# Performance work log

Measured on AMD Instinct MI355X. Metric: run time of the kernel, lower is better.

Reference implementation:

```python
import jax, jax.numpy as jnp
import numpy as np

B, N, T_IN, F_IN = 16, 30000, 6, 1
E = 120000          # edges per etype
N_ETYPES = 2        # etypes per graph (hg and tg each)
KT, LK = 3, 3
C1, C2 = 8, 11      # block channel sizes
HID = 128


def _conv2d(x, w, b):
    # x: [B,Cin,T,N], w: [Cout,Cin,kt,1] -> valid conv
    y = jax.lax.conv_general_dilated(x, w, window_strides=(1, 1), padding='VALID',
                                     dimension_numbers=('NCHW', 'OIHW', 'NCHW'))
    return y + b[None, :, None, None]


def _glu_tconv(x, w, b, c_out, x_align):
    # TemporalConvLayer with act='GLU'
    xc = _conv2d(x, w, b)
    return (xc[:, :c_out] + x_align) * jax.nn.sigmoid(xc[:, c_out:])


def _hetcheb(X, edges, W, bias):
    # Heterogeneous ChebConv (sum over edge types), lambda_max=2 => L_hat = -D^-1/2 A D^-1/2
    # X: [S,N,Cin], edges: [n_et,2,E] int32, W: [n_et,Lk,Cin,Cout], bias: [n_et,Cout]
    S, n, cin = X.shape
    Lk = W.shape[1]
    Xn = jnp.transpose(X, (1, 0, 2))  # [N,S,Cin]
    out = jnp.zeros((n, S, W.shape[-1]), X.dtype)
    for e in range(edges.shape[0]):
        src, dst = edges[e, 0], edges[e, 1]
        ones = jnp.ones(src.shape, X.dtype)
        deg_in = jnp.clip(jax.ops.segment_sum(ones, dst, num_segments=n), 1.0)
        deg_out = jnp.clip(jax.ops.segment_sum(ones, src, num_segments=n), 1.0)
        norm = jax.lax.rsqrt(deg_out)[src] * jax.lax.rsqrt(deg_in)[dst]  # [E]
        def prop(Tm):  # L_hat @ T = -(Ahat @ T); vectorized over all B*T slices at once
            Tf = Tm.reshape(n, S * cin)
            return -jax.ops.segment_sum(norm[:, None] * Tf[src], dst, num_segments=n).reshape(n, S, cin)
        Tkm2 = Xn
        Tkm1 = prop(Xn)
        z = jnp.einsum('nsc,cd->nsd', Tkm2, W[e, 0]) + jnp.einsum('nsc,cd->nsd', Tkm1, W[e, 1])
        for k in range(2, Lk):
            Tk = 2.0 * prop(Tkm1) - Tkm2
            z = z + jnp.einsum('nsc,cd->nsd', Tk, W[e, k])
            Tkm2, Tkm1 = Tkm1, Tk
        out = out + z + bias[e][None, None, :]
    return jnp.transpose(out, (1, 0, 2))  # [S,N,Cout]


def _block(x, hg_edges, tg_edges, align_fn, tw, tb, hW, hb, tW, tb2, c_out):
    # HetETAConvBlock (dropout = identity in eval)
    x_align = align_fn(x)[:, :, KT - 1:, :]
    x_t1 = _glu_tconv(x, tw, tb, c_out, x_align)          # [B,c_out,T',N]
    b_, c_, t_, n_ = x_t1.shape
    X = jnp.transpose(x_t1, (0, 2, 3, 1)).reshape(b_ * t_, n_, c_)  # batched slices
    xs = _hetcheb(X, hg_edges, hW, hb).reshape(b_, t_, n_, -1).transpose(0, 3, 1, 2)
    xt = _hetcheb(X, tg_edges, tW, tb2).reshape(b_, t_, n_, -1).transpose(0, 3, 1, 2)
    return jnp.concatenate([xs, xt], axis=1)              # [B,2*c_out,T',N]


def setup_inputs() -> dict:
    key = jax.random.key(0)
    ks = jax.random.split(key, 20)
    s = 0.1
    inp = {
        'x': jax.random.normal(ks[0], (B, N, T_IN, F_IN), jnp.float32),
        'hg_edges': jax.random.randint(ks[1], (N_ETYPES, 2, E), 0, N, jnp.int32),
        'tg_edges': jax.random.randint(ks[2], (N_ETYPES, 2, E), 0, N, jnp.int32),
        # block1: tconv GLU 1 -> 8 (out 2*8 channels)
        'tconv1_w': jax.random.normal(ks[3], (2 * C1, F_IN, KT, 1), jnp.float32) * s,
        'tconv1_b': jnp.zeros((2 * C1,), jnp.float32),
        'h1_W': jax.random.normal(ks[4], (N_ETYPES, LK, C1, C1), jnp.float32) * s,
        'h1_b': jnp.zeros((N_ETYPES, C1), jnp.float32),
        't1_W': jax.random.normal(ks[5], (N_ETYPES, LK, C1, C1), jnp.float32) * s,
        't1_b': jnp.zeros((N_ETYPES, C1), jnp.float32),
        # block2: align 16 -> 11 (conv1x1), tconv GLU 16 -> 11
        'align2_w': jax.random.normal(ks[6], (C2, 2 * C1, 1, 1), jnp.float32) * s,
        'align2_b': jnp.zeros((C2,), jnp.float32),
        'tconv2_w': jax.random.normal(ks[7], (2 * C2, 2 * C1, KT, 1), jnp.float32) * s,
        'tconv2_b': jnp.zeros((2 * C2,), jnp.float32),
        'h2_W': jax.random.normal(ks[8], (N_ETYPES, LK, C2, C2), jnp.float32) * s,
        'h2_b': jnp.zeros((N_ETYPES, C2), jnp.float32),
        't2_W': jax.random.normal(ks[9], (N_ETYPES, LK, C2, C2), jnp.float32) * s,
        't2_b': jnp.zeros((N_ETYPES, C2), jnp.float32),
        # output linear: 11*2*(6-2*(3-1)) = 44 -> HID
        'out_w': jax.random.normal(ks[10], (2 * C2 * (T_IN - 2 * (KT - 1)), HID), jnp.float32) * s,
        'out_b': jnp.zeros((HID,), jnp.float32),
    }
    return inp


def reference(x, hg_edges, tg_edges, tconv1_w, tconv1_b, h1_W, h1_b, t1_W, t1_b,
              align2_w, align2_b, tconv2_w, tconv2_b, h2_W, h2_b, t2_W, t2_b,
              out_w, out_b):
    x = jnp.transpose(x, (0, 3, 2, 1))  # [B,1,T,N]
    # block1: Align pads channels 1 -> 8
    align1 = lambda v: jnp.pad(v, ((0, 0), (0, C1 - F_IN), (0, 0), (0, 0)))
    x1 = _block(x, hg_edges, tg_edges, align1, tconv1_w, tconv1_b, h1_W, h1_b, t1_W, t1_b, C1)
    # block2: Align is 1x1 conv 16 -> 11
    align2 = lambda v: _conv2d(v, align2_w, align2_b)
    x2 = _block(x1, hg_edges, tg_edges, align2, tconv2_w, tconv2_b, h2_W, h2_b, t2_W, t2_b, C2)
    b_, c_, t_, n_ = x2.shape
    z = jnp.transpose(x2, (0, 3, 1, 2)).reshape(b_, n_, c_ * t_)  # [B,N,44]
    return z @ out_w + out_b  # [B,N,HID]
```

## Files before the change

kernel.cpp:

```cpp
#include <hip/hip_runtime.h>
#include <hip/hip_fp16.h>
#include <math.h>

#define EDGES 120000
#define NN    30000
#define NCH   118
#define T1SLOT 15360000

__device__ __forceinline__ float sigmoidf_(float x) { return 1.f / (1.f + __expf(-x)); }

union F4H8 { float4 v; __half h[8]; };
union F2H4 { float2 v; __half h[4]; };

__device__ __forceinline__ void unpack8(float4 v, float* f) {
  F4H8 u; u.v = v;
#pragma unroll
  for (int i = 0; i < 8; ++i) f[i] = __half2float(u.h[i]);
}
__device__ __forceinline__ float4 pack8(const float* f) {
  F4H8 u;
#pragma unroll
  for (int i = 0; i < 8; ++i) u.h[i] = __float2half(f[i]);
  return u.v;
}
__device__ __forceinline__ void unpack4(float2 v, float* f) {
  F2H4 u; u.v = v;
#pragma unroll
  for (int i = 0; i < 4; ++i) f[i] = __half2float(u.h[i]);
}
__device__ __forceinline__ float2 pack4(const float* f) {
  F2H4 u;
#pragma unroll
  for (int i = 0; i < 4; ++i) u.h[i] = __float2half(f[i]);
  return u.v;
}

#define CSR_STRIDE 270016
#define CSR_RP(base, l)   ((base) + (size_t)(l) * CSR_STRIDE)
#define CSR_PK(base, l)   ((const int2*)((base) + (size_t)(l) * CSR_STRIDE + 30016))
#define CSR_PKW(base, l)  ((int2*)((base) + (size_t)(l) * CSR_STRIDE + 30016))

__global__ void count_all_kernel(const int* __restrict__ hg, const int* __restrict__ tg,
                                 int* __restrict__ degO, int* __restrict__ degI) {
  int tid = blockIdx.x * blockDim.x + threadIdx.x;
  if (tid >= 4 * EDGES) return;
  int l = tid / EDGES, j = tid - l * EDGES;
  const int* G = (l < 2) ? hg : tg;
  const int* src = G + (size_t)(l & 1) * 2 * EDGES;
  const int* dst = src + EDGES;
  atomicAdd(&degO[l * NN + src[j]], 1);
  atomicAdd(&degI[l * NN + dst[j]], 1);
}

__global__ __launch_bounds__(256) void scan1_kernel(const int* __restrict__ degI,
                                                    int* __restrict__ csrBase,
                                                    int* __restrict__ partials) {
  int l = blockIdx.x / NCH, ch = blockIdx.x - l * NCH;
  int tid = threadIdx.x;
  int i = ch * 256 + tid;
  __shared__ int buf[256];
  int v = (i < NN) ? degI[l * NN + i] : 0;
  buf[tid] = v;
  __syncthreads();
  for (int off = 1; off < 256; off <<= 1) {
    int t = (tid >= off) ? buf[tid - off] : 0;
    __syncthreads();
    buf[tid] += t;
    __syncthreads();
  }
  int* rp = CSR_RP(csrBase, l);
  if (i < NN) rp[i + 1] = buf[tid];
  if (tid == 255) partials[l * NCH + ch] = buf[255];
}

__global__ __launch_bounds__(128) void scan2_kernel(int* __restrict__ partials) {
  __shared__ int buf[128];
  int tid = threadIdx.x;
  for (int l = 0; l < 4; ++l) {
    int v = (tid < NCH) ? partials[l * NCH + tid] : 0;
    buf[tid] = v;
    __syncthreads();
    for (int off = 1; off < 128; off <<= 1) {
      int t = (tid >= off) ? buf[tid - off] : 0;
      __syncthreads();
      buf[tid] += t;
      __syncthreads();
    }
    if (tid < NCH) partials[l * NCH + tid] = buf[tid] - v;
    __syncthreads();
  }
}

__global__ __launch_bounds__(256) void fixup_kernel(int* __restrict__ csrBase,
                                                    int* __restrict__ cursor,
                                                    const int* __restrict__ partials) {
  int l = blockIdx.x / NCH, ch = blockIdx.x - l * NCH;
  int i = ch * 256 + threadIdx.x;
  int* rp = CSR_RP(csrBase, l);
  int off = partials[l * NCH + ch];
  if (i < NN) {
    int val = rp[i + 1] + off;
    rp[i + 1] = val;
    if (i + 1 < NN) cursor[l * NN + i + 1] = val;
  }
  if (i == 0) { rp[0] = 0; cursor[l * NN] = 0; }
}

__global__ void fill_all_kernel(const int* __restrict__ hg, const int* __restrict__ tg,
                                const int* __restrict__ degO, const int* __restrict__ degI,
                                int* __restrict__ cursor, int* __restrict__ csrBase) {
  int tid = blockIdx.x * blockDim.x + threadIdx.x;
  if (tid >= 4 * EDGES) return;
  int l = tid / EDGES, j = tid - l * EDGES;
  const int* G = (l < 2) ? hg : tg;
  const int* src = G + (size_t)(l & 1) * 2 * EDGES;
  const int* dst = src + EDGES;
  int s = src[j], d = dst[j];
  int doo = degO[l * NN + s]; if (doo < 1) doo = 1;
  int dii = degI[l * NN + d]; if (dii < 1) dii = 1;
  float nm = rsqrtf((float)doo) * rsqrtf((float)dii);
  int p = atomicAdd(&cursor[l * NN + d], 1);
  CSR_PKW(csrBase, l)[p] = make_int2(s, __float_as_int(nm));
}

__global__ void glu1_kernel(const float* __restrict__ x, const float* __restrict__ w,
                            const float* __restrict__ b, __half* __restrict__ X1h) {
  int idx = blockIdx.x * blockDim.x + threadIdx.x;
  if (idx >= NN * 64) return;
  int n = idx >> 6, s = idx & 63;
  int bb = s >> 2, t = s & 3;
  const float* xb = x + ((long)bb * NN + n) * 6;
  float x0 = xb[t], x1 = xb[t + 1], x2 = xb[t + 2];
  float o[8];
#pragma unroll
  for (int c = 0; c < 8; ++c) {
    float p = w[c * 3 + 0] * x0 + w[c * 3 + 1] * x1 + w[c * 3 + 2] * x2 + b[c];
    float q = w[(c + 8) * 3 + 0] * x0 + w[(c + 8) * 3 + 1] * x1 + w[(c + 8) * 3 + 2] * x2 + b[c + 8];
    float al = (c == 0) ? x2 : 0.f;
    o[c] = (p + al) * sigmoidf_(q);
  }
  reinterpret_cast<float4*>(X1h)[idx] = pack8(o);
}

__global__ __launch_bounds__(256) void pull1_kernel(const int* __restrict__ csrBase,
                                                    const __half* __restrict__ Xh,
                                                    __half* __restrict__ T1hAll) {
  int gtid = blockIdx.x * 256 + threadIdx.x;
  int l = gtid / (NN * 64);
  int t = gtid - l * (NN * 64);
  int n = t >> 6, j = t & 63;
  const int* rp = CSR_RP(csrBase, l);
  const int2* pk = CSR_PK(csrBase, l);
  const float4* in4 = reinterpret_cast<const float4*>(Xh);
  float acc[8];
#pragma unroll
  for (int i = 0; i < 8; ++i) acc[i] = 0.f;
  int e = rp[n], end = rp[n + 1];
  for (; e + 4 <= end; e += 4) {
    int2 p0 = pk[e], p1 = pk[e + 1], p2 = pk[e + 2], p3 = pk[e + 3];
    float4 v0 = in4[(long)p0.x * 64 + j];
    float4 v1 = in4[(long)p1.x * 64 + j];
    float4 v2 = in4[(long)p2.x * 64 + j];
    float4 v3 = in4[(long)p3.x * 64 + j];
    float f[8];
    float n0 = __int_as_float(p0.y), n1 = __int_as_float(p1.y);
    float n2 = __int_as_float(p2.y), n3 = __int_as_float(p3.y);
    unpack8(v0, f);
#pragma unroll
    for (int i = 0; i < 8; ++i) acc[i] -= n0 * f[i];
    unpack8(v1, f);
#pragma unroll
    for (int i = 0; i < 8; ++i) acc[i] -= n1 * f[i];
    unpack8(v2, f);
#pragma unroll
    for (int i = 0; i < 8; ++i) acc[i] -= n2 * f[i];
    unpack8(v3, f);
#pragma unroll
    for (int i = 0; i < 8; ++i) acc[i] -= n3 * f[i];
  }
  for (; e < end; ++e) {
    int2 p = pk[e];
    float4 v = in4[(long)p.x * 64 + j];
    float nm = __int_as_float(p.y);
    float f[8];
    unpack8(v, f);
#pragma unroll
    for (int i = 0; i < 8; ++i) acc[i] -= nm * f[i];
  }
  reinterpret_cast<float4*>(T1hAll)[(size_t)l * (T1SLOT / 8) + t] = pack8(acc);
}

__global__ __launch_bounds__(256) void cheb1_kernel(const int* __restrict__ csrBase,
    const __half* __restrict__ Xh, const __half* __restrict__ T1hAll,
    const float* __restrict__ Whg, const float* __restrict__ bhg,
    const float* __restrict__ Wtg, const float* __restrict__ btg,
    __half* __restrict__ Pbase) {
  constexpr int C = 8, CC = 64;
  __shared__ float wx[CC], w1[CC], w2[CC], bs[C];
  int gtid = blockIdx.x * 256 + threadIdx.x;
  int l = gtid / (NN * 64);
  int tid = gtid - l * (NN * 64);
  int g = l >> 1, et = l & 1;
  const float* W = (g ? Wtg : Whg) + et * 3 * CC;
  const float* bias = (g ? btg : bhg) + et * C;
  for (int i = threadIdx.x; i < CC; i += 256) {
    float w0v = W[i], w1v = W[CC + i], w2v = W[2 * CC + i];
    wx[i] = w0v - w2v; w1[i] = w1v; w2[i] = -2.f * w2v;
  }
  if (threadIdx.x < C) bs[threadIdx.x] = bias[threadIdx.x];
  __syncthreads();
  int n = tid >> 6, s = tid & 63;
  const int* rp = CSR_RP(csrBase, l);
  const int2* pk = CSR_PK(csrBase, l);
  const float4* T4 = reinterpret_cast<const float4*>(T1hAll + (size_t)l * T1SLOT);
  float acc[C];
#pragma unroll
  for (int c = 0; c < C; ++c) acc[c] = 0.f;
  int e = rp[n], end = rp[n + 1];
  for (; e + 4 <= end; e += 4) {
    int2 p0 = pk[e], p1 = pk[e + 1], p2 = pk[e + 2], p3 = pk[e + 3];
    float4 v0 = T4[(long)p0.x * 64 + s];
    float4 v1 = T4[(long)p1.x * 64 + s];
    float4 v2 = T4[(long)p2.x * 64 + s];
    float4 v3 = T4[(long)p3.x * 64 + s];
    float n0 = __int_as_float(p0.y), n1 = __int_as_float(p1.y);
    float n2 = __int_as_float(p2.y), n3 = __int_as_float(p3.y);
    float f[8];
    unpack8(v0, f);
#pragma unroll
    for (int c = 0; c < C; ++c) acc[c] += n0 * f[c];
    unpack8(v1, f);
#pragma unroll
    for (int c = 0; c < C; ++c) acc[c] += n1 * f[c];
    unpack8(v2, f);
#pragma unroll
    for (int c = 0; c < C; ++c) acc[c] += n2 * f[c];
    unpack8(v3, f);
#pragma unroll
    for (int c = 0; c < C; ++c) acc[c] += n3 * f[c];
  }
  for (; e < end; ++e) {
    int2 p = pk[e];
    float4 v = T4[(long)p.x * 64 + s];
    float nm = __int_as_float(p.y);
    float f[8];
    unpack8(v, f);
#pragma unroll
    for (int c = 0; c < C; ++c) acc[c] += nm * f[c];
  }
  float xv[C], tv[C];
  unpack8(reinterpret_cast<const float4*>(Xh)[tid], xv);
  unpack8(T4[tid], tv);
  float z[C];
#pragma unroll
  for (int d = 0; d < C; ++d) z[d] = bs[d];
#pragma unroll
  for (int c = 0; c < C; ++c) {
    float xc = xv[c], tc = tv[c], ac = acc[c];
#pragma unroll
    for (int d = 0; d < C; ++d)
      z[d] += xc * wx[c * C + d] + tc * w1[c * C + d] + ac * w2[c * C + d];
  }
  reinterpret_cast<float4*>(Pbase)[(size_t)l * (T1SLOT / 8) + tid] = pack8(z);
}

__global__ __launch_bounds__(256) void glu2_kernel(const __half* __restrict__ P,
                                                   const float* __restrict__ w2, const float* __restrict__ b2,
                                                   const float* __restrict__ aw, const float* __restrict__ ab,
                                                   __half* __restrict__ X2nh) {
  __shared__ float w2s[22 * 16 * 3], b2s[22], aws[11 * 16], abs_[11];
  for (int i = threadIdx.x; i < 22 * 16 * 3; i += 256) w2s[i] = w2[i];
  if (threadIdx.x < 22) b2s[threadIdx.x] = b2[threadIdx.x];
  for (int i = threadIdx.x; i < 11 * 16; i += 256) aws[i] = aw[i];
  if (threadIdx.x < 11) abs_[threadIdx.x] = ab[threadIdx.x];
  __syncthreads();
  int idx = blockIdx.x * 256 + threadIdx.x;
  int n = idx >> 5, s = idx & 31;
  int bb = s >> 1, t = s & 1;
  long rbase = (long)n * 64 + bb * 4 + t;
  const float4* H0 = reinterpret_cast<const float4*>(P) + rbase;
  const float4* H1 = reinterpret_cast<const float4*>(P + (size_t)T1SLOT) + rbase;
  const float4* Ta = reinterpret_cast<const float4*>(P + 2 * (size_t)T1SLOT) + rbase;
  const float4* Tb = reinterpret_cast<const float4*>(P + 3 * (size_t)T1SLOT) + rbase;
  float hv[24], tv[24], tmp[8];
#pragma unroll
  for (int q = 0; q < 3; ++q) {
    unpack8(H0[q], hv + 8 * q); unpack8(H1[q], tmp);
#pragma unroll
    for (int i = 0; i < 8; ++i) hv[8 * q + i] += tmp[i];
    unpack8(Ta[q], tv + 8 * q); unpack8(Tb[q], tmp);
#pragma unroll
    for (int i = 0; i < 8; ++i) tv[8 * q + i] += tmp[i];
  }
  float o[12];
  o[11] = 0.f;
#pragma unroll
  for (int co = 0; co < 11; ++co) {
    float p = b2s[co], q = b2s[co + 11], a = abs_[co];
#pragma unroll
    for (int ci = 0; ci < 16; ++ci) {
      float v0 = (ci < 8) ? hv[ci] : tv[ci - 8];
      float v1 = (ci < 8) ? hv[8 + ci] : tv[ci];
      float v2 = (ci < 8) ? hv[16 + ci] : tv[8 + ci];
      p += w2s[(co * 16 + ci) * 3 + 0] * v0 + w2s[(co * 16 + ci) * 3 + 1] * v1 +
           w2s[(co * 16 + ci) * 3 + 2] * v2;
      q += w2s[((co + 11) * 16 + ci) * 3 + 0] * v0 + w2s[((co + 11) * 16 + ci) * 3 + 1] * v1 +
           w2s[((co + 11) * 16 + ci) * 3 + 2] * v2;
      a += aws[co * 16 + ci] * v2;
    }
    o[co] = (p + a) * sigmoidf_(q);
  }
  float2* o2 = reinterpret_cast<float2*>(X2nh) + (long)idx * 3;
  o2[0] = pack4(o);
  o2[1] = pack4(o + 4);
  o2[2] = pack4(o + 8);
}

__global__ __launch_bounds__(256) void pull2_kernel(const int* __restrict__ csrBase,
                                                    const __half* __restrict__ Xh,
                                                    __half* __restrict__ T1hAll) {
  int gtid = blockIdx.x * 256 + threadIdx.x;
  int l = gtid / (NN * 96);
  int t = gtid - l * (NN * 96);
  int n = t / 96, j = t - n * 96;
  const int* rp = CSR_RP(csrBase, l);
  const int2* pk = CSR_PK(csrBase, l);
  const float2* in2 = reinterpret_cast<const float2*>(Xh);
  float acc[4];
#pragma unroll
  for (int i = 0; i < 4; ++i) acc[i] = 0.f;
  int e = rp[n], end = rp[n + 1];
  for (; e + 4 <= end; e += 4) {
    int2 p0 = pk[e], p1 = pk[e + 1], p2 = pk[e + 2], p3 = pk[e + 3];
    float2 v0 = in2[(long)p0.x * 96 + j];
    float2 v1 = in2[(long)p1.x * 96 + j];
    float2 v2 = in2[(long)p2.x * 96 + j];
    float2 v3 = in2[(long)p3.x * 96 + j];
    float f[4];
    float n0 = __int_as_float(p0.y), n1 = __int_as_float(p1.y);
    float n2 = __int_as_float(p2.y), n3 = __int_as_float(p3.y);
    unpack4(v0, f);
#pragma unroll
    for (int i = 0; i < 4; ++i) acc[i] -= n0 * f[i];
    unpack4(v1, f);
#pragma unroll
    for (int i = 0; i < 4; ++i) acc[i] -= n1 * f[i];
    unpack4(v2, f);
#pragma unroll
    for (int i = 0; i < 4; ++i) acc[i] -= n2 * f[i];
    unpack4(v3, f);
#pragma unroll
    for (int i = 0; i < 4; ++i) acc[i] -= n3 * f[i];
  }
  for (; e < end; ++e) {
    int2 p = pk[e];
    float2 v = in2[(long)p.x * 96 + j];
    float nm = __int_as_float(p.y);
    float f[4];
    unpack4(v, f);
#pragma unroll
    for (int i = 0; i < 4; ++i) acc[i] -= nm * f[i];
  }
  reinterpret_cast<float2*>(T1hAll)[(size_t)l * (T1SLOT / 4) + t] = pack4(acc);
}

__global__ __launch_bounds__(256) void cheb2_kernel(const int* __restrict__ csrBase,
    const __half* __restrict__ Xh, const __half* __restrict__ T1hAll,
    const float* __restrict__ Whg, const float* __restrict__ bhg,
    const float* __restrict__ Wtg, const float* __restrict__ btg,
    __half* __restrict__ Pbase) {
  constexpr int C = 11, CC = 121;
  __shared__ float wx[CC], w1[CC], w2[CC], bs[C];
  int gtid = blockIdx.x * 256 + threadIdx.x;
  int l = gtid / (NN * 32);
  int tid = gtid - l * (NN * 32);
  int g = l >> 1, et = l & 1;
  const float* W = (g ? Wtg : Whg) + et * 3 * CC;
  const float* bias = (g ? btg : bhg) + et * C;
  for (int i = threadIdx.x; i < CC; i += 256) {
    float w0v = W[i], w1v = W[CC + i], w2v = W[2 * CC + i];
    wx[i] = w0v - w2v; w1[i] = w1v; w2[i] = -2.f * w2v;
  }
  if (threadIdx.x < C) bs[threadIdx.x] = bias[threadIdx.x];
  __syncthreads();
  int n = tid >> 5, s = tid & 31;
  int s3 = s * 3;
  const int* rp = CSR_RP(csrBase, l);
  const int2* pk = CSR_PK(csrBase, l);
  const float2* A2v = reinterpret_cast<const float2*>(T1hAll + (size_t)l * T1SLOT);
  float acc[12];
#pragma unroll
  for (int c = 0; c < 12; ++c) acc[c] = 0.f;
  int e = rp[n], end = rp[n + 1];
  for (; e + 4 <= end; e += 4) {
    int2 p0 = pk[e], p1 = pk[e + 1], p2 = pk[e + 2], p3 = pk[e + 3];
    long r0 = (long)p0.x * 96 + s3, r1 = (long)p1.x * 96 + s3;
    long r2 = (long)p2.x * 96 + s3, r3 = (long)p3.x * 96 + s3;
    float2 a0 = A2v[r0], a1 = A2v[r0 + 1], a2 = A2v[r0 + 2];
    float2 b0 = A2v[r1], b1 = A2v[r1 + 1], b2 = A2v[r1 + 2];
    float2 c0 = A2v[r2], c1 = A2v[r2 + 1], c2 = A2v[r2 + 2];
    float2 d0 = A2v[r3], d1 = A2v[r3 + 1], d2 = A2v[r3 + 2];
    float n0 = __int_as_float(p0.y), n1 = __int_as_float(p1.y);
    float n2 = __int_as_float(p2.y), n3 = __int_as_float(p3.y);
    float f[4];
    unpack4(a0, f);
#pragma unroll
    for (int i = 0; i < 4; ++i) acc[i] += n0 * f[i];
    unpack4(a1, f);
#pragma unroll
    for (int i = 0; i < 4; ++i) acc[4 + i] += n0 * f[i];
    unpack4(a2, f);
#pragma unroll
    for (int i = 0; i < 4; ++i) acc[8 + i] += n0 * f[i];
    unpack4(b0, f);
#pragma unroll
    for (int i = 0; i < 4; ++i) acc[i] += n1 * f[i];
    unpack4(b1, f);
#pragma unroll
    for (int i = 0; i < 4; ++i) acc[4 + i] += n1 * f[i];
    unpack4(b2, f);
#pragma unroll
    for (int i = 0; i < 4; ++i) acc[8 + i] += n1 * f[i];
    unpack4(c0, f);
#pragma unroll
    for (int i = 0; i < 4; ++i) acc[i] += n2 * f[i];
    unpack4(c1, f);
#pragma unroll
    for (int i = 0; i < 4; ++i) acc[4 + i] += n2 * f[i];
    unpack4(c2, f);
#pragma unroll
    for (int i = 0; i < 4; ++i) acc[8 + i] += n2 * f[i];
    unpack4(d0, f);
#pragma unroll
    for (int i = 0; i < 4; ++i) acc[i] += n3 * f[i];
    unpack4(d1, f);
#pragma unroll
    for (int i = 0; i < 4; ++i) acc[4 + i] += n3 * f[i];
    unpack4(d2, f);
#pragma unroll
    for (int i = 0; i < 4; ++i) acc[8 + i] += n3 * f[i];
  }
  for (; e < end; ++e) {
    int2 p = pk[e];
    long r = (long)p.x * 96 + s3;
    float2 a0 = A2v[r], a1 = A2v[r + 1], a2 = A2v[r + 2];
    float nm = __int_as_float(p.y);
    float f[4];
    unpack4(a0, f);
#pragma unroll
    for (int i = 0; i < 4; ++i) acc[i] += nm * f[i];
    unpack4(a1, f);
#pragma unroll
    for (int i = 0; i < 4; ++i) acc[4 + i] += nm * f[i];
    unpack4(a2, f);
#pragma unroll
    for (int i = 0; i < 4; ++i) acc[8 + i] += nm * f[i];
  }
  float z[12];
#pragma unroll
  for (int d = 0; d < C; ++d) z[d] = bs[d];
  z[11] = 0.f;
  const float2* X2v = reinterpret_cast<const float2*>(Xh);
  long own = (long)tid * 3;
#pragma unroll
  for (int q = 0; q < 3; ++q) {
    float xv[4], tv[4];
    unpack4(X2v[own + q], xv);
    unpack4(A2v[own + q], tv);
#pragma unroll
    for (int k = 0; k < 4; ++k) {
      int c = q * 4 + k;
      if (c == 11) continue;
      float xc = xv[k], tc = tv[k], ac = acc[c];
#pragma unroll
      for (int d = 0; d < C; ++d)
        z[d] += xc * wx[c * C + d] + tc * w1[c * C + d] + ac * w2[c * C + d];
    }
  }
  float2* o2 = reinterpret_cast<float2*>(Pbase) + (size_t)l * (T1SLOT / 4) + (long)tid * 3;
  o2[0] = pack4(z);
  o2[1] = pack4(z + 4);
  o2[2] = pack4(z + 8);
}

__global__ __launch_bounds__(256) void final_kernel(const __half* __restrict__ Pbase,
                                                    const float* __restrict__ W, const float* __restrict__ bias,
                                                    float* __restrict__ out) {
  __shared__ __half zsr[64][48];
  int tid = threadIdx.x;
  long r0 = (long)blockIdx.x * 64;
#pragma unroll
  for (int it = 0; it < 2; ++it) {
    int item = it * 256 + tid;
    if (item < 384) {
      int row = item / 6, piece = item - row * 6;
      long r = r0 + row;
      int b = (int)(r / NN), n = (int)(r - (long)b * NN);
      int sp = (piece < 3) ? 0 : 2;
      int f4i = (piece < 3) ? piece : piece - 3;
      const float4* sA = reinterpret_cast<const float4*>(Pbase + (size_t)sp * T1SLOT);
      const float4* sB = reinterpret_cast<const float4*>(Pbase + (size_t)(sp + 1) * T1SLOT);
      long idx = (long)n * 48 + b * 3 + f4i;
      float fa[8], fb[8];
      unpack8(sA[idx], fa);
      unpack8(sB[idx], fb);
#pragma unroll
      for (int i = 0; i < 8; ++i) fa[i] += fb[i];
      *reinterpret_cast<float4*>(&zsr[row][(piece < 3 ? 0 : 24) + f4i * 8]) = pack8(fa);
    }
  }
  int c = tid & 127, h = tid >> 7;
  float wp[48];
#pragma unroll
  for (int off = 0; off < 48; ++off) {
    int half_ = off / 24, r_ = off - half_ * 24;
    int t = r_ / 12, c_ = r_ - t * 12;
    wp[off] = (c_ == 11) ? 0.f : W[(2 * (c_ + half_ * 11) + t) * 128 + c];
  }
  float bh = bias[c];
  __syncthreads();
  int rbeg = h * 32;
#pragma unroll 2
  for (int row = rbeg; row < rbeg + 32; ++row) {
    const float4* zr4 = reinterpret_cast<const float4*>(&zsr[row][0]);
    float acc = bh;
#pragma unroll
    for (int q = 0; q < 6; ++q) {
      F4H8 u; u.v = zr4[q];
#pragma unroll
      for (int i = 0; i < 8; ++i)
        acc = fmaf(__half2float(u.h[i]), wp[q * 8 + i], acc);
    }
    out[(r0 + row) * 128 + c] = acc;
  }
}

extern "C" void kernel_launch(void* const* d_in, const int* in_sizes, int n_in,
                              void* d_out, int out_size, void* d_ws, size_t ws_size,
                              hipStream_t stream) {
  const float* x    = (const float*)d_in[0];
  const int*   hg   = (const int*)d_in[1];
  const int*   tg   = (const int*)d_in[2];
  const float* t1w  = (const float*)d_in[3];
  const float* t1b  = (const float*)d_in[4];
  const float* h1W  = (const float*)d_in[5];
  const float* h1b  = (const float*)d_in[6];
  const float* g1W  = (const float*)d_in[7];
  const float* g1b  = (const float*)d_in[8];
  const float* a2w  = (const float*)d_in[9];
  const float* a2b  = (const float*)d_in[10];
  const float* t2w  = (const float*)d_in[11];
  const float* t2b  = (const float*)d_in[12];
  const float* h2W  = (const float*)d_in[13];
  const float* h2b  = (const float*)d_in[14];
  const float* g2W  = (const float*)d_in[15];
  const float* g2b  = (const float*)d_in[16];
  const float* outw = (const float*)d_in[17];
  const float* outb = (const float*)d_in[18];
  float* out = (float*)d_out;

  __half* T1h = (__half*)d_ws;
  __half* Xh  = T1h + 4L * T1SLOT;
  __half* P   = Xh + T1SLOT;
  int* csrBase  = (int*)(P + 4L * T1SLOT);
  int* degO     = csrBase + 4 * CSR_STRIDE;
  int* degI     = degO + 4 * NN;
  int* cursor   = degI + 4 * NN;
  int* partials = cursor + 4 * NN;

  hipMemsetAsync(degO, 0, 8 * NN * sizeof(int), stream);
  count_all_kernel<<<(4 * EDGES + 255) / 256, 256, 0, stream>>>(hg, tg, degO, degI);
  scan1_kernel<<<4 * NCH, 256, 0, stream>>>(degI, csrBase, partials);
  scan2_kernel<<<1, 128, 0, stream>>>(partials);
  fixup_kernel<<<4 * NCH, 256, 0, stream>>>(csrBase, cursor, partials);
  fill_all_kernel<<<(4 * EDGES + 255) / 256, 256, 0, stream>>>(hg, tg, degO, degI, cursor, csrBase);

  glu1_kernel<<<NN * 64 / 256, 256, 0, stream>>>(x, t1w, t1b, Xh);
  pull1_kernel<<<4 * NN * 64 / 256, 256, 0, stream>>>(csrBase, Xh, T1h);
  cheb1_kernel<<<4 * NN * 64 / 256, 256, 0, stream>>>(csrBase, Xh, T1h, h1W, h1b, g1W, g1b, P);

  glu2_kernel<<<NN * 32 / 256, 256, 0, stream>>>(P, t2w, t2b, a2w, a2b, Xh);
  pull2_kernel<<<4 * NN * 96 / 256, 256, 0, stream>>>(csrBase, Xh, T1h);
  cheb2_kernel<<<4 * NN * 32 / 256, 256, 0, stream>>>(csrBase, Xh, T1h, h2W, h2b, g2W, g2b, P);

  final_kernel<<<7500, 256, 0, stream>>>(P, outw, outb, out);
}
```

Measured before the change: 899.0 us.

## Split cheb kernels per layer launch and make final kernel persistent

The fused cheb1/cheb2 kernels that covered all four graph-etype layers are replaced by four separate launches, one per layer, with CSR pointers and weights chosen on the host. This removes the per-thread layer division and index arithmetic. The final projection kernel becomes grid-stride over tiles with 1024 blocks, so the 48 weight values are loaded into registers once per block instead of once per tile. The degree scratch buffers move into the P region, which is overwritten later; this adds launches and relies on that aliasing being safe.

```diff
diff --git a/kernel.cpp b/kernel.cpp
--- a/kernel.cpp
+++ b/kernel.cpp
@@ -190,29 +190,21 @@
   reinterpret_cast<float4*>(T1hAll)[(size_t)l * (T1SLOT / 8) + t] = pack8(acc);
 }
 
-__global__ __launch_bounds__(256) void cheb1_kernel(const int* __restrict__ csrBase,
-    const __half* __restrict__ Xh, const __half* __restrict__ T1hAll,
-    const float* __restrict__ Whg, const float* __restrict__ bhg,
-    const float* __restrict__ Wtg, const float* __restrict__ btg,
-    __half* __restrict__ Pbase) {
+__global__ __launch_bounds__(256) void cheb1_kernel(const int* __restrict__ rp, const int2* __restrict__ pk,
+    const __half* __restrict__ Xh, const __half* __restrict__ T1l,
+    const float* __restrict__ W, const float* __restrict__ bias,
+    __half* __restrict__ Pl) {
   constexpr int C = 8, CC = 64;
   __shared__ float wx[CC], w1[CC], w2[CC], bs[C];
-  int gtid = blockIdx.x * 256 + threadIdx.x;
-  int l = gtid / (NN * 64);
-  int tid = gtid - l * (NN * 64);
-  int g = l >> 1, et = l & 1;
-  const float* W = (g ? Wtg : Whg) + et * 3 * CC;
-  const float* bias = (g ? btg : bhg) + et * C;
   for (int i = threadIdx.x; i < CC; i += 256) {
     float w0v = W[i], w1v = W[CC + i], w2v = W[2 * CC + i];
     wx[i] = w0v - w2v; w1[i] = w1v; w2[i] = -2.f * w2v;
   }
   if (threadIdx.x < C) bs[threadIdx.x] = bias[threadIdx.x];
   __syncthreads();
+  int tid = blockIdx.x * 256 + threadIdx.x;
   int n = tid >> 6, s = tid & 63;
-  const int* rp = CSR_RP(csrBase, l);
-  const int2* pk = CSR_PK(csrBase, l);
-  const float4* T4 = reinterpret_cast<const float4*>(T1hAll + (size_t)l * T1SLOT);
+  const float4* T4 = reinterpret_cast<const float4*>(T1l);
   float acc[C];
 #pragma unroll
   for (int c = 0; c < C; ++c) acc[c] = 0.f;
@@ -261,7 +253,7 @@
     for (int d = 0; d < C; ++d)
       z[d] += xc * wx[c * C + d] + tc * w1[c * C + d] + ac * w2[c * C + d];
   }
-  reinterpret_cast<float4*>(Pbase)[(size_t)l * (T1SLOT / 8) + tid] = pack8(z);
+  reinterpret_cast<float4*>(Pl)[tid] = pack8(z);
 }
 
 __global__ __launch_bounds__(256) void glu2_kernel(const __half* __restrict__ P,
@@ -364,30 +356,22 @@
   reinterpret_cast<float2*>(T1hAll)[(size_t)l * (T1SLOT / 4) + t] = pack4(acc);
 }
 
-__global__ __launch_bounds__(256) void cheb2_kernel(const int* __restrict__ csrBase,
-    const __half* __restrict__ Xh, const __half* __restrict__ T1hAll,
-    const float* __restrict__ Whg, const float* __restrict__ bhg,
-    const float* __restrict__ Wtg, const float* __restrict__ btg,
-    __half* __restrict__ Pbase) {
+__global__ __launch_bounds__(256) void cheb2_kernel(const int* __restrict__ rp, const int2* __restrict__ pk,
+    const __half* __restrict__ Xh, const __half* __restrict__ T1l,
+    const float* __restrict__ W, const float* __restrict__ bias,
+    __half* __restrict__ P2l) {
   constexpr int C = 11, CC = 121;
   __shared__ float wx[CC], w1[CC], w2[CC], bs[C];
-  int gtid = blockIdx.x * 256 + threadIdx.x;
-  int l = gtid / (NN * 32);
-  int tid = gtid - l * (NN * 32);
-  int g = l >> 1, et = l & 1;
-  const float* W = (g ? Wtg : Whg) + et * 3 * CC;
-  const float* bias = (g ? btg : bhg) + et * C;
   for (int i = threadIdx.x; i < CC; i += 256) {
     float w0v = W[i], w1v = W[CC + i], w2v = W[2 * CC + i];
     wx[i] = w0v - w2v; w1[i] = w1v; w2[i] = -2.f * w2v;
   }
   if (threadIdx.x < C) bs[threadIdx.x] = bias[threadIdx.x];
   __syncthreads();
+  int tid = blockIdx.x * 256 + threadIdx.x;
   int n = tid >> 5, s = tid & 31;
   int s3 = s * 3;
-  const int* rp = CSR_RP(csrBase, l);
-  const int2* pk = CSR_PK(csrBase, l);
-  const float2* A2v = reinterpret_cast<const float2*>(T1hAll + (size_t)l * T1SLOT);
+  const float2* A2v = reinterpret_cast<const float2*>(T1l);
   float acc[12];
 #pragma unroll
   for (int c = 0; c < 12; ++c) acc[c] = 0.f;
@@ -477,7 +461,7 @@
         z[d] += xc * wx[c * C + d] + tc * w1[c * C + d] + ac * w2[c * C + d];
     }
   }
-  float2* o2 = reinterpret_cast<float2*>(Pbase) + (size_t)l * (T1SLOT / 4) + (long)tid * 3;
+  float2* o2 = reinterpret_cast<float2*>(P2l) + (long)tid * 3;
   o2[0] = pack4(z);
   o2[1] = pack4(z + 4);
   o2[2] = pack4(z + 8);
@@ -488,27 +472,6 @@
                                                     float* __restrict__ out) {
   __shared__ __half zsr[64][48];
   int tid = threadIdx.x;
-  long r0 = (long)blockIdx.x * 64;
-#pragma unroll
-  for (int it = 0; it < 2; ++it) {
-    int item = it * 256 + tid;
-    if (item < 384) {
-      int row = item / 6, piece = item - row * 6;
-      long r = r0 + row;
-      int b = (int)(r / NN), n = (int)(r - (long)b * NN);
-      int sp = (piece < 3) ? 0 : 2;
-      int f4i = (piece < 3) ? piece : piece - 3;
-      const float4* sA = reinterpret_cast<const float4*>(Pbase + (size_t)sp * T1SLOT);
-      const float4* sB = reinterpret_cast<const float4*>(Pbase + (size_t)(sp + 1) * T1SLOT);
-      long idx = (long)n * 48 + b * 3 + f4i;
-      float fa[8], fb[8];
-      unpack8(sA[idx], fa);
-      unpack8(sB[idx], fb);
-#pragma unroll
-      for (int i = 0; i < 8; ++i) fa[i] += fb[i];
-      *reinterpret_cast<float4*>(&zsr[row][(piece < 3 ? 0 : 24) + f4i * 8]) = pack8(fa);
-    }
-  }
   int c = tid & 127, h = tid >> 7;
   float wp[48];
 #pragma unroll
@@ -518,20 +481,44 @@
     wp[off] = (c_ == 11) ? 0.f : W[(2 * (c_ + half_ * 11) + t) * 128 + c];
   }
   float bh = bias[c];
-  __syncthreads();
-  int rbeg = h * 32;
+  for (int tile = blockIdx.x; tile < 7500; tile += gridDim.x) {
+    long r0 = (long)tile * 64;
+    __syncthreads();
+#pragma unroll
+    for (int it = 0; it < 2; ++it) {
+      int item = it * 256 + tid;
+      if (item < 384) {
+        int row = item / 6, piece = item - row * 6;
+        long r = r0 + row;
+        int b = (int)(r / NN), n = (int)(r - (long)b * NN);
+        int sp = (piece < 3) ? 0 : 2;
+        int f4i = (piece < 3) ? piece : piece - 3;
+        const float4* sA = reinterpret_cast<const float4*>(Pbase + (size_t)sp * T1SLOT);
+        const float4* sB = reinterpret_cast<const float4*>(Pbase + (size_t)(sp + 1) * T1SLOT);
+        long idx = (long)n * 48 + b * 3 + f4i;
+        float fa[8], fb[8];
+        unpack8(sA[idx], fa);
+        unpack8(sB[idx], fb);
+#pragma unroll
+        for (int i = 0; i < 8; ++i) fa[i] += fb[i];
+        *reinterpret_cast<float4*>(&zsr[row][(piece < 3 ? 0 : 24) + f4i * 8]) = pack8(fa);
+      }
+    }
+    __syncthreads();
+    int rbeg = h * 32;
 #pragma unroll 2
-  for (int row = rbeg; row < rbeg + 32; ++row) {
-    const float4* zr4 = reinterpret_cast<const float4*>(&zsr[row][0]);
-    float acc = bh;
-#pragma unroll
-    for (int q = 0; q < 6; ++q) {
-      F4H8 u; u.v = zr4[q];
-#pragma unroll
-      for (int i = 0; i < 8; ++i)
-        acc = fmaf(__half2float(u.h[i]), wp[q * 8 + i], acc);
+    for (int row = rbeg; row < rbeg + 32; ++row) {
+      const float4* zr4 = reinterpret_cast<const float4*>(&zsr[row][0]);
+      float acc = bh;
+#pragma unroll
+      for (int q = 0; q < 6; ++q) {
+        F4H8 u; u.v = zr4[q];
+#pragma unroll
+        for (int i = 0; i < 8; ++i)
+          acc = fmaf(__half2float(u.h[i]), wp[q * 8 + i], acc);
+      }
+      out[(r0 + row) * 128 + c] = acc;
     }
-    out[(r0 + row) * 128 + c] = acc;
   }
 }
 
@@ -563,7 +550,7 @@
   __half* Xh  = T1h + 4L * T1SLOT;
   __half* P   = Xh + T1SLOT;
   int* csrBase  = (int*)(P + 4L * T1SLOT);
-  int* degO     = csrBase + 4 * CSR_STRIDE;
+  int* degO     = (int*)P;
   int* degI     = degO + 4 * NN;
   int* cursor   = degI + 4 * NN;
   int* partials = cursor + 4 * NN;
@@ -577,11 +564,23 @@
 
   glu1_kernel<<<NN * 64 / 256, 256, 0, stream>>>(x, t1w, t1b, Xh);
   pull1_kernel<<<4 * NN * 64 / 256, 256, 0, stream>>>(csrBase, Xh, T1h);
-  cheb1_kernel<<<4 * NN * 64 / 256, 256, 0, stream>>>(csrBase, Xh, T1h, h1W, h1b, g1W, g1b, P);
+  for (int l = 0; l < 4; ++l) {
+    const float* W1 = ((l < 2) ? h1W : g1W) + (size_t)(l & 1) * 3 * 64;
+    const float* b1 = ((l < 2) ? h1b : g1b) + (size_t)(l & 1) * 8;
+    cheb1_kernel<<<NN * 64 / 256, 256, 0, stream>>>(CSR_RP(csrBase, l), CSR_PK(csrBase, l),
+                                                    Xh, T1h + (size_t)l * T1SLOT, W1, b1,
+                                                    P + (size_t)l * T1SLOT);
+  }
 
   glu2_kernel<<<NN * 32 / 256, 256, 0, stream>>>(P, t2w, t2b, a2w, a2b, Xh);
   pull2_kernel<<<4 * NN * 96 / 256, 256, 0, stream>>>(csrBase, Xh, T1h);
-  cheb2_kernel<<<4 * NN * 32 / 256, 256, 0, stream>>>(csrBase, Xh, T1h, h2W, h2b, g2W, g2b, P);
-
-  final_kernel<<<7500, 256, 0, stream>>>(P, outw, outb, out);
-}
+  for (int l = 0; l < 4; ++l) {
+    const float* W2 = ((l < 2) ? h2W : g2W) + (size_t)(l & 1) * 3 * 121;
+    const float* b2 = ((l < 2) ? h2b : g2b) + (size_t)(l & 1) * 11;
+    cheb2_kernel<<<NN * 32 / 256, 256, 0, stream>>>(CSR_RP(csrBase, l), CSR_PK(csrBase, l),
+                                                    Xh, T1h + (size_t)l * T1SLOT, W2, b2,
+                                                    P + (size_t)l * T1SLOT);
+  }
+
+  final_kernel<<<1024, 256, 0, stream>>>(P, outw, outb, out);
+}
```

Result: slower. 958.1 us (+6.6%).
